# Performance work log

Measured on AMD Instinct MI355X. Metric: run time of the kernel, lower is better.

Reference implementation:

```python
import jax, jax.numpy as jnp
import numpy as np

# Hyperparameters matching init_kwargs
LR = 0.02
AT = 0.3
DSBETA = 0.1
EPS_DS = 0.5

B, D, N = 8192, 1024, 4096


def setup_inputs() -> dict:
    key = jax.random.key(0)
    k0, k1, k2, k3 = jax.random.split(key, 4)
    x = jax.random.normal(k0, (B, D), dtype=jnp.float32)
    weights = jax.random.normal(k1, (N, D), dtype=jnp.float32)
    relevance = jax.random.uniform(k2, (N, D), dtype=jnp.float32)
    moving_avg = jax.random.uniform(k3, (N, D), dtype=jnp.float32)
    node_control = jnp.ones((N,), dtype=jnp.float32)
    return {"x": x, "weights": weights, "relevance": relevance,
            "moving_avg": moving_avg, "node_control": node_control}


def reference(x, weights, relevance, moving_avg, node_control):
    n, d = weights.shape
    # pairwise squared distances [B, N] via one GEMM
    x2 = jnp.sum(x * x, axis=1, keepdims=True)            # [B,1]
    w2 = jnp.sum(weights * weights, axis=1)[None, :]      # [1,N]
    dists = x2 + w2 - 2.0 * jnp.matmul(x, weights.T)      # [B,N]
    # weighted_distance + activation
    rsum = jnp.sum(relevance, axis=1)                     # [N]
    dw = dists * (rsum / d)[None, :]
    dw = jnp.where(jnp.isnan(dw), 0.0, dw)
    act = (rsum[None, :] / (rsum[None, :] + dw + 1e-7)) * node_control[None, :]
    act_max = jnp.max(act, axis=1)                        # [B]
    idx = jnp.argmax(act, axis=1)                         # [B] winner per sample
    # high-activation mask; group samples by winner node (unique_node_diff_vectorized
    # == per-node mean of assigned high samples, done with segment_sum at fixed N)
    high = (act_max >= AT).astype(x.dtype)                # [B]
    counts = jax.ops.segment_sum(high, idx, num_segments=n)               # [N]
    sums = jax.ops.segment_sum(x * high[:, None], idx, num_segments=n)    # [N,D]
    has = (counts > 0).astype(x.dtype)[:, None]           # [N,1] nodes with >=1 high sample
    mean_s = sums / jnp.maximum(counts, 1.0)[:, None]     # [N,D] updatable_samples (dense)
    # update_node math (EMA moving_avg -> relevance -> weight update)
    a = LR * DSBETA
    distance = jnp.abs(mean_s - weights)
    mavg_new = a * distance + (1.0 - a) * moving_avg
    mx = jnp.max(mavg_new, axis=1, keepdims=True)
    mn = jnp.min(mavg_new, axis=1, keepdims=True)
    avg = jnp.mean(mavg_new, axis=1, keepdims=True)
    rel_new = 1.0 / (1.0 + jnp.exp((mavg_new - avg) / (EPS_DS * (mx - mn))))
    rel_new = jnp.where(jnp.isnan(rel_new), 1.0, rel_new)
    w_new = weights + LR * (mean_s - weights)
    # Original returns rows only for unique winning nodes (dynamic shape); here we
    # return fixed-shape [N,D] arrays masked to zero for nodes with no high sample.
    return (mean_s * has, w_new * has, rel_new * has)
```

## Files before the change

kernel.cpp:

```cpp
#include <hip/hip_runtime.h>
#include <stdint.h>

#define B_DIM 8192
#define D_DIM 1024
#define N_DIM 4096
#define ND ((size_t)N_DIM * D_DIM)
#define LRc 0.02f
#define ATc 0.3f
#define EMAc (0.02f * 0.1f)
#define QS 32.0f
#define INV_QS2 (1.0f / (QS * QS))
#define MARGIN_G 8.0f

typedef int intv4 __attribute__((ext_vector_type(4)));

__device__ __forceinline__ void async16(void* lds, const void* g) {
    __builtin_amdgcn_global_load_lds((const __attribute__((address_space(1))) void*)g,
                                     (__attribute__((address_space(3))) void*)lds, 16, 0, 0);
}

__device__ __forceinline__ int q8(float v) {
    return (int)rintf(fminf(fmaxf(v * QS, -127.0f), 127.0f));
}

__global__ __launch_bounds__(256) void prep(const float* __restrict__ x, const float* __restrict__ w,
                                            const float* __restrict__ rel,
                                            signed char* __restrict__ xq, signed char* __restrict__ wq,
                                            float* __restrict__ x2, float* __restrict__ w2,
                                            float* __restrict__ rsum, float* __restrict__ gb) {
    const int t = threadIdx.x;
    __shared__ float r1[4], r2s[4];
    if (blockIdx.x < B_DIM) {
        const int b = blockIdx.x;
        const float4 v = ((const float4*)(x + (size_t)b * D_DIM))[t];
        float ss = v.x * v.x + v.y * v.y + v.z * v.z + v.w * v.w;
        unsigned pk = (unsigned)(q8(v.x) & 255) | ((unsigned)(q8(v.y) & 255) << 8)
                    | ((unsigned)(q8(v.z) & 255) << 16) | ((unsigned)(q8(v.w) & 255) << 24);
        ((unsigned*)(xq + (size_t)b * D_DIM))[t] = pk;
#pragma unroll
        for (int o = 32; o; o >>= 1) ss += __shfl_xor(ss, o);
        if ((t & 63) == 0) r1[t >> 6] = ss;
        __syncthreads();
        if (t == 0) x2[b] = r1[0] + r1[1] + r1[2] + r1[3];
    } else {
        const int n = blockIdx.x - B_DIM;
        const float4 v = ((const float4*)(w + (size_t)n * D_DIM))[t];
        const float4 rv = ((const float4*)(rel + (size_t)n * D_DIM))[t];
        float ss = v.x * v.x + v.y * v.y + v.z * v.z + v.w * v.w;
        float rs = rv.x + rv.y + rv.z + rv.w;
        unsigned pk = (unsigned)(q8(v.x) & 255) | ((unsigned)(q8(v.y) & 255) << 8)
                    | ((unsigned)(q8(v.z) & 255) << 16) | ((unsigned)(q8(v.w) & 255) << 24);
        ((unsigned*)(wq + (size_t)n * D_DIM))[t] = pk;
#pragma unroll
        for (int o = 32; o; o >>= 1) { ss += __shfl_xor(ss, o); rs += __shfl_xor(rs, o); }
        if ((t & 63) == 0) { r1[t >> 6] = ss; r2s[t >> 6] = rs; }
        __syncthreads();
        if (t == 0) {
            const float w2v = r1[0] + r1[1] + r1[2] + r1[3];
            const float rsv = r2s[0] + r2s[1] + r2s[2] + r2s[3];
            w2[n] = w2v;
            rsum[n] = rsv;
            gb[n] = w2v + (1e-7f * (float)D_DIM) / rsv;
        }
    }
}

__global__ __launch_bounds__(256) void gemm_g(const signed char* __restrict__ xq,
                                              const signed char* __restrict__ wq,
                                              const float* __restrict__ gb,
                                              unsigned short* __restrict__ gq,
                                              unsigned short* __restrict__ tmin) {
    __shared__ int4 As[1024];
    __shared__ int4 Bs[1024];
    const int t = threadIdx.x;
    const int mt = blockIdx.x & 63;
    const int nt = blockIdx.x >> 6;
    const int m0 = mt * 128, n0 = nt * 128;
    const int lane = t & 63, wave = t >> 6;
    const int q = lane >> 4, ln = lane & 15;
    const int wm = wave >> 1, wn = wave & 1;

    intv4 acc[4][4];
#pragma unroll
    for (int i = 0; i < 4; ++i)
#pragma unroll
        for (int j = 0; j < 4; ++j) acc[i][j] = (intv4){0, 0, 0, 0};

    int rr[4], jj[4];
#pragma unroll
    for (int it = 0; it < 4; ++it) {
        int L = t + it * 256;
        rr[it] = L >> 3;
        jj[it] = (L & 7) ^ (rr[it] & 7);
    }

    const signed char* Ap = xq + (size_t)m0 * D_DIM;
    const signed char* Bp = wq + (size_t)n0 * D_DIM;
    for (int kt = 0; kt < 8; ++kt) {
        const int k0 = kt * 128;
#pragma unroll
        for (int it = 0; it < 4; ++it) {
            int L = t + it * 256;
            async16((char*)As + L * 16, Ap + (size_t)rr[it] * D_DIM + k0 + jj[it] * 16);
            async16((char*)Bs + L * 16, Bp + (size_t)rr[it] * D_DIM + k0 + jj[it] * 16);
        }
        __syncthreads();
#pragma unroll
        for (int ks = 0; ks < 2; ++ks) {
            intv4 a[4], b[4];
#pragma unroll
            for (int i = 0; i < 4; ++i) {
                int r = wm * 64 + i * 16 + ln;
                int jx = (ks * 4 + q) ^ (r & 7);
                a[i] = *(const intv4*)((const char*)As + (r * 8 + jx) * 16);
            }
#pragma unroll
            for (int i = 0; i < 4; ++i) {
                int r = wn * 64 + i * 16 + ln;
                int jx = (ks * 4 + q) ^ (r & 7);
                b[i] = *(const intv4*)((const char*)Bs + (r * 8 + jx) * 16);
            }
#pragma unroll
            for (int i = 0; i < 4; ++i)
#pragma unroll
                for (int j = 0; j < 4; ++j)
                    acc[i][j] = __builtin_amdgcn_mfma_i32_16x16x64_i8(a[i], b[j], acc[i][j], 0, 0, 0);
        }
        __syncthreads();
    }

    float gbv[4];
#pragma unroll
    for (int jt = 0; jt < 4; ++jt) gbv[jt] = gb[n0 + wn * 64 + jt * 16 + ln];
    const float cf = 2.0f * INV_QS2;
#pragma unroll
    for (int i = 0; i < 4; ++i) {
#pragma unroll
        for (int r = 0; r < 4; ++r) {
            const int m = m0 + wm * 64 + i * 16 + q * 4 + r;
            float gmin = 3.4e38f;
#pragma unroll
            for (int jt = 0; jt < 4; ++jt) {
                const float g = gbv[jt] - cf * (float)acc[i][jt][r];
                gmin = fminf(gmin, g);
                gq[(size_t)m * N_DIM + n0 + wn * 64 + jt * 16 + ln] = (unsigned short)__builtin_bit_cast(short, (_Float16)g);
            }
#pragma unroll
            for (int o = 1; o < 16; o <<= 1) gmin = fminf(gmin, __shfl_xor(gmin, o));
            if (ln == 0)
                tmin[(size_t)m * 64 + nt * 2 + wn] = (unsigned short)__builtin_bit_cast(short, (_Float16)gmin);
        }
    }
}

__global__ __launch_bounds__(256) void resolve(const unsigned short* __restrict__ gq,
                                               const unsigned short* __restrict__ tmin,
                                               const float* __restrict__ x, const float* __restrict__ w,
                                               const float* __restrict__ w2, const float* __restrict__ rsum,
                                               const float* __restrict__ ncp,
                                               int* __restrict__ win) {
    const int lane = threadIdx.x & 63, wave = threadIdx.x >> 6;
    const int b = blockIdx.x * 4 + wave;
    const float4* xr = (const float4*)(x + (size_t)b * D_DIM);
    float4 xv[4];
#pragma unroll
    for (int j = 0; j < 4; ++j) xv[j] = xr[lane + j * 64];
    float px2 = 0.f;
#pragma unroll
    for (int j = 0; j < 4; ++j)
        px2 += xv[j].x * xv[j].x + xv[j].y * xv[j].y + xv[j].z * xv[j].z + xv[j].w * xv[j].w;
    float tv = (float)__builtin_bit_cast(_Float16, (short)tmin[(size_t)b * 64 + lane]);
    float rowmin = tv;
#pragma unroll
    for (int o = 32; o; o >>= 1) {
        rowmin = fminf(rowmin, __shfl_xor(rowmin, o));
        px2 += __shfl_xor(px2, o);
    }
    const float x2v = px2;
    const float th = rowmin + MARGIN_G;

    float best_act = -1.0f;
    int best_n = N_DIM;
    unsigned long long tmask = __ballot(tv <= th);
    while (tmask) {
        const int tt = __ffsll((long long)tmask) - 1;
        tmask &= tmask - 1;
        const float gv = (float)__builtin_bit_cast(_Float16, (short)gq[(size_t)b * N_DIM + tt * 64 + lane]);
        unsigned long long cmask = __ballot(gv <= th);
        while (cmask) {
            const int l = __ffsll((long long)cmask) - 1;
            cmask &= cmask - 1;
            const int n = tt * 64 + l;
            const float4* wr = (const float4*)(w + (size_t)n * D_DIM);
            float p = 0.f;
#pragma unroll
            for (int j = 0; j < 4; ++j) {
                const float4 wv = wr[lane + j * 64];
                p += xv[j].x * wv.x + xv[j].y * wv.y + xv[j].z * wv.z + xv[j].w * wv.w;
            }
#pragma unroll
            for (int o = 32; o; o >>= 1) p += __shfl_xor(p, o);
            const float dist = x2v + w2[n] - 2.0f * p;
            const float rs = rsum[n];
            const float dw = dist * rs * (1.0f / (float)D_DIM);
            const float a = rs * ncp[n] / (rs + dw + 1e-7f);
            if (a > best_act || (a == best_act && n < best_n)) { best_act = a; best_n = n; }
        }
    }
    if (lane == 0) win[b] = (best_act >= ATc) ? best_n : -1;
}

__global__ __launch_bounds__(256) void finalize(const float* __restrict__ x, const float* __restrict__ w,
                                                const float* __restrict__ mavg, const int* __restrict__ win,
                                                float* __restrict__ out) {
    const int n = blockIdx.x, t = threadIdx.x;
    __shared__ unsigned short list[B_DIM];
    __shared__ int cnt;
    if (t == 0) cnt = 0;
    __syncthreads();
    const int4* wp = (const int4*)win;
#pragma unroll
    for (int k = 0; k < 8; ++k) {
        const int4 v = wp[k * 256 + t];
        const int b0 = (k * 256 + t) * 4;
        if (v.x == n) list[atomicAdd(&cnt, 1)] = (unsigned short)(b0 + 0);
        if (v.y == n) list[atomicAdd(&cnt, 1)] = (unsigned short)(b0 + 1);
        if (v.z == n) list[atomicAdd(&cnt, 1)] = (unsigned short)(b0 + 2);
        if (v.w == n) list[atomicAdd(&cnt, 1)] = (unsigned short)(b0 + 3);
    }
    __syncthreads();
    const int c = cnt;
    float4 s = {0.f, 0.f, 0.f, 0.f};
    for (int e = 0; e < c; ++e) {
        const float4 xv = ((const float4*)(x + (size_t)list[e] * D_DIM))[t];
        s.x += xv.x; s.y += xv.y; s.z += xv.z; s.w += xv.w;
    }
    const float has = (c > 0) ? 1.0f : 0.0f;
    const float invc = 1.0f / fmaxf((float)c, 1.0f);
    const size_t base4 = (size_t)n * (D_DIM / 4);
    const float4 wv = ((const float4*)w)[base4 + t];
    const float4 mk = ((const float4*)mavg)[base4 + t];
    float4 ms, mv;
    ms.x = s.x * invc; ms.y = s.y * invc; ms.z = s.z * invc; ms.w = s.w * invc;
    mv.x = EMAc * fabsf(ms.x - wv.x) + (1.0f - EMAc) * mk.x;
    mv.y = EMAc * fabsf(ms.y - wv.y) + (1.0f - EMAc) * mk.y;
    mv.z = EMAc * fabsf(ms.z - wv.z) + (1.0f - EMAc) * mk.z;
    mv.w = EMAc * fabsf(ms.w - wv.w) + (1.0f - EMAc) * mk.w;
    float lmax = fmaxf(fmaxf(mv.x, mv.y), fmaxf(mv.z, mv.w));
    float lmin = fminf(fminf(mv.x, mv.y), fminf(mv.z, mv.w));
    float lsum = mv.x + mv.y + mv.z + mv.w;
#pragma unroll
    for (int o = 32; o; o >>= 1) {
        lmax = fmaxf(lmax, __shfl_xor(lmax, o));
        lmin = fminf(lmin, __shfl_xor(lmin, o));
        lsum += __shfl_xor(lsum, o);
    }
    __shared__ float smax[4], smin[4], ssum[4];
    const int wave = t >> 6, lane = t & 63;
    if (lane == 0) { smax[wave] = lmax; smin[wave] = lmin; ssum[wave] = lsum; }
    __syncthreads();
    const float mx = fmaxf(fmaxf(smax[0], smax[1]), fmaxf(smax[2], smax[3]));
    const float mn = fminf(fminf(smin[0], smin[1]), fminf(smin[2], smin[3]));
    const float avg = (ssum[0] + ssum[1] + ssum[2] + ssum[3]) * (1.0f / (float)D_DIM);
    const float scale = 0.5f * (mx - mn);
    const float invs = (scale > 0.0f) ? 1.0f / scale : 0.0f;
    float4 relv;
    if (scale > 0.0f) {
        relv.x = 1.0f / (1.0f + __expf((mv.x - avg) * invs));
        relv.y = 1.0f / (1.0f + __expf((mv.y - avg) * invs));
        relv.z = 1.0f / (1.0f + __expf((mv.z - avg) * invs));
        relv.w = 1.0f / (1.0f + __expf((mv.w - avg) * invs));
    } else {
        relv.x = relv.y = relv.z = relv.w = 1.0f;
    }
    float4* o0 = (float4*)out;
    float4 r0, r1, r2;
    r0.x = ms.x * has; r0.y = ms.y * has; r0.z = ms.z * has; r0.w = ms.w * has;
    r1.x = (wv.x + LRc * (ms.x - wv.x)) * has;
    r1.y = (wv.y + LRc * (ms.y - wv.y)) * has;
    r1.z = (wv.z + LRc * (ms.z - wv.z)) * has;
    r1.w = (wv.w + LRc * (ms.w - wv.w)) * has;
    r2.x = relv.x * has; r2.y = relv.y * has; r2.z = relv.z * has; r2.w = relv.w * has;
    o0[base4 + t] = r0;
    o0[ND / 4 + base4 + t] = r1;
    o0[2 * (ND / 4) + base4 + t] = r2;
}

extern "C" void kernel_launch(void* const* d_in, const int* in_sizes, int n_in,
                              void* d_out, int out_size, void* d_ws, size_t ws_size,
                              hipStream_t stream) {
    const float* x    = (const float*)d_in[0];
    const float* w    = (const float*)d_in[1];
    const float* rel  = (const float*)d_in[2];
    const float* mavg = (const float*)d_in[3];
    const float* nc   = (const float*)d_in[4];
    float* out = (float*)d_out;

    char* p = (char*)d_ws;
    size_t off = 0;
    auto take = [&](size_t bytes) -> char* {
        char* r = p + off;
        off += (bytes + 255) & ~(size_t)255;
        return r;
    };
    signed char* xq = (signed char*)take((size_t)B_DIM * D_DIM);
    signed char* wq = (signed char*)take((size_t)N_DIM * D_DIM);
    float* x2       = (float*)take((size_t)B_DIM * 4);
    float* w2       = (float*)take((size_t)N_DIM * 4);
    float* rsum     = (float*)take((size_t)N_DIM * 4);
    float* gb       = (float*)take((size_t)N_DIM * 4);
    unsigned short* gq   = (unsigned short*)take((size_t)B_DIM * N_DIM * 2);
    unsigned short* tmin = (unsigned short*)take((size_t)B_DIM * 64 * 2);
    int* win        = (int*)take((size_t)B_DIM * 4);

    prep<<<B_DIM + N_DIM, 256, 0, stream>>>(x, w, rel, xq, wq, x2, w2, rsum, gb);
    gemm_g<<<2048, 256, 0, stream>>>(xq, wq, gb, gq, tmin);
    resolve<<<B_DIM / 4, 256, 0, stream>>>(gq, tmin, x, w, w2, rsum, nc, win);
    finalize<<<N_DIM, 256, 0, stream>>>(x, w, mavg, win, out);
}
```

Baseline: 213.5 us.

## Widen GEMM tile, store 8-bit residuals over tile minima, skip recheck for single candidates

```diff
diff --git a/kernel.cpp b/kernel.cpp
--- a/kernel.cpp
+++ b/kernel.cpp
@@ -10,7 +10,7 @@
 #define EMAc (0.02f * 0.1f)
 #define QS 32.0f
 #define INV_QS2 (1.0f / (QS * QS))
-#define MARGIN_G 8.0f
+#define MARGIN_G 10.0f
 
 typedef int intv4 __attribute__((ext_vector_type(4)));
 
@@ -65,33 +65,37 @@
     }
 }
 
-__global__ __launch_bounds__(256) void gemm_g(const signed char* __restrict__ xq,
-                                              const signed char* __restrict__ wq,
-                                              const float* __restrict__ gb,
-                                              unsigned short* __restrict__ gq,
-                                              unsigned short* __restrict__ tmin) {
+__global__ __launch_bounds__(256, 2) void gemm_g(const signed char* __restrict__ xq,
+                                                 const signed char* __restrict__ wq,
+                                                 const float* __restrict__ gb,
+                                                 unsigned char* __restrict__ res,
+                                                 float* __restrict__ tminp) {
     __shared__ int4 As[1024];
-    __shared__ int4 Bs[1024];
+    __shared__ int4 Bs[2048];
     const int t = threadIdx.x;
     const int mt = blockIdx.x & 63;
     const int nt = blockIdx.x >> 6;
-    const int m0 = mt * 128, n0 = nt * 128;
+    const int m0 = mt * 128, n0 = nt * 256;
     const int lane = t & 63, wave = t >> 6;
     const int q = lane >> 4, ln = lane & 15;
     const int wm = wave >> 1, wn = wave & 1;
 
-    intv4 acc[4][4];
+    intv4 acc[4][8];
 #pragma unroll
     for (int i = 0; i < 4; ++i)
 #pragma unroll
-        for (int j = 0; j < 4; ++j) acc[i][j] = (intv4){0, 0, 0, 0};
-
-    int rr[4], jj[4];
+        for (int j = 0; j < 8; ++j) acc[i][j] = (intv4){0, 0, 0, 0};
+
+    int rrA[4], jjA[4], rrB[8], jjB[8];
 #pragma unroll
     for (int it = 0; it < 4; ++it) {
         int L = t + it * 256;
-        rr[it] = L >> 3;
-        jj[it] = (L & 7) ^ (rr[it] & 7);
+        rrA[it] = L >> 3; jjA[it] = (L & 7) ^ (rrA[it] & 7);
+    }
+#pragma unroll
+    for (int it = 0; it < 8; ++it) {
+        int L = t + it * 256;
+        rrB[it] = L >> 3; jjB[it] = (L & 7) ^ (rrB[it] & 7);
     }
 
     const signed char* Ap = xq + (size_t)m0 * D_DIM;
@@ -99,15 +103,15 @@
     for (int kt = 0; kt < 8; ++kt) {
         const int k0 = kt * 128;
 #pragma unroll
-        for (int it = 0; it < 4; ++it) {
-            int L = t + it * 256;
-            async16((char*)As + L * 16, Ap + (size_t)rr[it] * D_DIM + k0 + jj[it] * 16);
-            async16((char*)Bs + L * 16, Bp + (size_t)rr[it] * D_DIM + k0 + jj[it] * 16);
-        }
+        for (int it = 0; it < 4; ++it)
+            async16((char*)As + (t + it * 256) * 16, Ap + (size_t)rrA[it] * D_DIM + k0 + jjA[it] * 16);
+#pragma unroll
+        for (int it = 0; it < 8; ++it)
+            async16((char*)Bs + (t + it * 256) * 16, Bp + (size_t)rrB[it] * D_DIM + k0 + jjB[it] * 16);
         __syncthreads();
 #pragma unroll
         for (int ks = 0; ks < 2; ++ks) {
-            intv4 a[4], b[4];
+            intv4 a[4], b[8];
 #pragma unroll
             for (int i = 0; i < 4; ++i) {
                 int r = wm * 64 + i * 16 + ln;
@@ -115,99 +119,129 @@
                 a[i] = *(const intv4*)((const char*)As + (r * 8 + jx) * 16);
             }
 #pragma unroll
-            for (int i = 0; i < 4; ++i) {
-                int r = wn * 64 + i * 16 + ln;
+            for (int j = 0; j < 8; ++j) {
+                int r = wn * 128 + j * 16 + ln;
                 int jx = (ks * 4 + q) ^ (r & 7);
-                b[i] = *(const intv4*)((const char*)Bs + (r * 8 + jx) * 16);
+                b[j] = *(const intv4*)((const char*)Bs + (r * 8 + jx) * 16);
             }
 #pragma unroll
             for (int i = 0; i < 4; ++i)
 #pragma unroll
-                for (int j = 0; j < 4; ++j)
+                for (int j = 0; j < 8; ++j)
                     acc[i][j] = __builtin_amdgcn_mfma_i32_16x16x64_i8(a[i], b[j], acc[i][j], 0, 0, 0);
         }
         __syncthreads();
     }
 
-    float gbv[4];
-#pragma unroll
-    for (int jt = 0; jt < 4; ++jt) gbv[jt] = gb[n0 + wn * 64 + jt * 16 + ln];
+    float gbv[8];
+#pragma unroll
+    for (int j = 0; j < 8; ++j) gbv[j] = gb[n0 + wn * 128 + j * 16 + ln];
     const float cf = 2.0f * INV_QS2;
 #pragma unroll
     for (int i = 0; i < 4; ++i) {
 #pragma unroll
         for (int r = 0; r < 4; ++r) {
             const int m = m0 + wm * 64 + i * 16 + q * 4 + r;
-            float gmin = 3.4e38f;
-#pragma unroll
-            for (int jt = 0; jt < 4; ++jt) {
-                const float g = gbv[jt] - cf * (float)acc[i][jt][r];
-                gmin = fminf(gmin, g);
-                gq[(size_t)m * N_DIM + n0 + wn * 64 + jt * 16 + ln] = (unsigned short)__builtin_bit_cast(short, (_Float16)g);
-            }
-#pragma unroll
-            for (int o = 1; o < 16; o <<= 1) gmin = fminf(gmin, __shfl_xor(gmin, o));
-            if (ln == 0)
-                tmin[(size_t)m * 64 + nt * 2 + wn] = (unsigned short)__builtin_bit_cast(short, (_Float16)gmin);
-        }
-    }
-}
-
-__global__ __launch_bounds__(256) void resolve(const unsigned short* __restrict__ gq,
-                                               const unsigned short* __restrict__ tmin,
+            float g[8];
+            float mnA = 3.4e38f, mnB = 3.4e38f;
+#pragma unroll
+            for (int j = 0; j < 8; ++j) {
+                g[j] = gbv[j] - cf * (float)acc[i][j][r];
+                if (j < 4) mnA = fminf(mnA, g[j]); else mnB = fminf(mnB, g[j]);
+            }
+#pragma unroll
+            for (int o = 1; o < 16; o <<= 1) {
+                mnA = fminf(mnA, __shfl_xor(mnA, o));
+                mnB = fminf(mnB, __shfl_xor(mnB, o));
+            }
+            if (ln == 0) {
+                tminp[(size_t)m * 64 + nt * 4 + wn * 2 + 0] = mnA;
+                tminp[(size_t)m * 64 + nt * 4 + wn * 2 + 1] = mnB;
+            }
+#pragma unroll
+            for (int j = 0; j < 8; ++j) {
+                const float base = (j < 4) ? mnA : mnB;
+                int u = (int)rintf((g[j] - base) * 2.0f);
+                u = (u > 255) ? 255 : u;
+                res[(size_t)m * N_DIM + n0 + wn * 128 + j * 16 + ln] = (unsigned char)u;
+            }
+        }
+    }
+}
+
+__global__ __launch_bounds__(256) void resolve(const unsigned char* __restrict__ res,
+                                               const float* __restrict__ tminp,
+                                               const float* __restrict__ x2p,
                                                const float* __restrict__ x, const float* __restrict__ w,
                                                const float* __restrict__ w2, const float* __restrict__ rsum,
                                                const float* __restrict__ ncp,
                                                int* __restrict__ win) {
     const int lane = threadIdx.x & 63, wave = threadIdx.x >> 6;
     const int b = blockIdx.x * 4 + wave;
-    const float4* xr = (const float4*)(x + (size_t)b * D_DIM);
-    float4 xv[4];
-#pragma unroll
-    for (int j = 0; j < 4; ++j) xv[j] = xr[lane + j * 64];
-    float px2 = 0.f;
-#pragma unroll
-    for (int j = 0; j < 4; ++j)
-        px2 += xv[j].x * xv[j].x + xv[j].y * xv[j].y + xv[j].z * xv[j].z + xv[j].w * xv[j].w;
-    float tv = (float)__builtin_bit_cast(_Float16, (short)tmin[(size_t)b * 64 + lane]);
+    const float tv = tminp[(size_t)b * 64 + lane];
     float rowmin = tv;
 #pragma unroll
-    for (int o = 32; o; o >>= 1) {
-        rowmin = fminf(rowmin, __shfl_xor(rowmin, o));
-        px2 += __shfl_xor(px2, o);
-    }
-    const float x2v = px2;
+    for (int o = 32; o; o >>= 1) rowmin = fminf(rowmin, __shfl_xor(rowmin, o));
     const float th = rowmin + MARGIN_G;
-
-    float best_act = -1.0f;
-    int best_n = N_DIM;
-    unsigned long long tmask = __ballot(tv <= th);
-    while (tmask) {
-        const int tt = __ffsll((long long)tmask) - 1;
-        tmask &= tmask - 1;
-        const float gv = (float)__builtin_bit_cast(_Float16, (short)gq[(size_t)b * N_DIM + tt * 64 + lane]);
-        unsigned long long cmask = __ballot(gv <= th);
-        while (cmask) {
-            const int l = __ffsll((long long)cmask) - 1;
-            cmask &= cmask - 1;
-            const int n = tt * 64 + l;
-            const float4* wr = (const float4*)(w + (size_t)n * D_DIM);
-            float p = 0.f;
-#pragma unroll
-            for (int j = 0; j < 4; ++j) {
-                const float4 wv = wr[lane + j * 64];
-                p += xv[j].x * wv.x + xv[j].y * wv.y + xv[j].z * wv.z + xv[j].w * wv.w;
-            }
-#pragma unroll
-            for (int o = 32; o; o >>= 1) p += __shfl_xor(p, o);
-            const float dist = x2v + w2[n] - 2.0f * p;
-            const float rs = rsum[n];
-            const float dw = dist * rs * (1.0f / (float)D_DIM);
-            const float a = rs * ncp[n] / (rs + dw + 1e-7f);
-            if (a > best_act || (a == best_act && n < best_n)) { best_act = a; best_n = n; }
-        }
-    }
-    if (lane == 0) win[b] = (best_act >= ATc) ? best_n : -1;
+    const unsigned long long tmask = __ballot(tv <= th);
+    const float x2v = x2p[b];
+
+    int cnt = 0, myn = -1;
+    float myg = 0.0f;
+    unsigned long long tm = tmask;
+    while (tm) {
+        const int tt = __ffsll((long long)tm) - 1;
+        tm &= tm - 1;
+        const float tb = __shfl(tv, tt);
+        const unsigned char rv = res[(size_t)b * N_DIM + tt * 64 + lane];
+        const float g = tb + 0.5f * (float)rv;
+        const bool c = (g <= th);
+        cnt += __popcll(__ballot(c));
+        if (c && myn < 0) { myn = tt * 64 + lane; myg = g; }
+    }
+
+    if (cnt == 1) {
+        if (myn >= 0) {
+            const float act = ncp[myn] * (float)D_DIM / ((float)D_DIM + x2v + myg);
+            win[b] = (act >= ATc) ? myn : -1;
+        }
+    } else {
+        const float4* xr = (const float4*)(x + (size_t)b * D_DIM);
+        float4 xv[4];
+#pragma unroll
+        for (int j = 0; j < 4; ++j) xv[j] = xr[lane + j * 64];
+        float best_act = -1.0f;
+        int best_n = N_DIM;
+        tm = tmask;
+        while (tm) {
+            const int tt = __ffsll((long long)tm) - 1;
+            tm &= tm - 1;
+            const float tb = __shfl(tv, tt);
+            const unsigned char rv = res[(size_t)b * N_DIM + tt * 64 + lane];
+            const float g = tb + 0.5f * (float)rv;
+            unsigned long long cm = __ballot(g <= th);
+            while (cm) {
+                const int l = __ffsll((long long)cm) - 1;
+                cm &= cm - 1;
+                const int n = tt * 64 + l;
+                const float4* wr = (const float4*)(w + (size_t)n * D_DIM);
+                float p = 0.f;
+#pragma unroll
+                for (int j = 0; j < 4; ++j) {
+                    const float4 wv = wr[lane + j * 64];
+                    p += xv[j].x * wv.x + xv[j].y * wv.y + xv[j].z * wv.z + xv[j].w * wv.w;
+                }
+#pragma unroll
+                for (int o = 32; o; o >>= 1) p += __shfl_xor(p, o);
+                const float dist = x2v + w2[n] - 2.0f * p;
+                const float rs = rsum[n];
+                const float dw = dist * rs * (1.0f / (float)D_DIM);
+                const float a = rs * ncp[n] / (rs + dw + 1e-7f);
+                if (a > best_act || (a == best_act && n < best_n)) { best_act = a; best_n = n; }
+            }
+        }
+        if (lane == 0) win[b] = (best_act >= ATc) ? best_n : -1;
+    }
 }
 
 __global__ __launch_bounds__(256) void finalize(const float* __restrict__ x, const float* __restrict__ w,
@@ -309,12 +343,12 @@
     float* w2       = (float*)take((size_t)N_DIM * 4);
     float* rsum     = (float*)take((size_t)N_DIM * 4);
     float* gb       = (float*)take((size_t)N_DIM * 4);
-    unsigned short* gq   = (unsigned short*)take((size_t)B_DIM * N_DIM * 2);
-    unsigned short* tmin = (unsigned short*)take((size_t)B_DIM * 64 * 2);
+    unsigned char* res = (unsigned char*)take((size_t)B_DIM * N_DIM);
+    float* tminp    = (float*)take((size_t)B_DIM * 64 * 4);
     int* win        = (int*)take((size_t)B_DIM * 4);
 
     prep<<<B_DIM + N_DIM, 256, 0, stream>>>(x, w, rel, xq, wq, x2, w2, rsum, gb);
-    gemm_g<<<2048, 256, 0, stream>>>(xq, wq, gb, gq, tmin);
-    resolve<<<B_DIM / 4, 256, 0, stream>>>(gq, tmin, x, w, w2, rsum, nc, win);
+    gemm_g<<<1024, 256, 0, stream>>>(xq, wq, gb, res, tminp);
+    resolve<<<B_DIM / 4, 256, 0, stream>>>(res, tminp, x2, x, w, w2, rsum, nc, win);
     finalize<<<N_DIM, 256, 0, stream>>>(x, w, mavg, win, out);
 }
```

Measured after the change: 205.6 us. -3.7%, faster.
